# Optimization experiments

Hardware: AMD Instinct MI355X
Metric: run time of the kernel (lower is better)

Reference implementation:

```python
import jax, jax.numpy as jnp
import numpy as np

V, E, H, L, B, S = 50000, 512, 512, 2, 4, 256
DIN = 2 * E  # == 2*H, layer input size for all layers
GH = 4 * H   # torch LSTM gate order: i, f, g, o


def _lstm_dir(x, mask, w_ih, w_hh, b, reverse):
    """One direction of one LSTM layer with packed-sequence semantics.
    x: [B,S,DIN], mask: [B,S] bool. Returns [B,S,H]; padded steps emit 0
    and do not update state (matches pack_padded/pad_packed behavior)."""
    xs = jnp.swapaxes(x, 0, 1)                      # [S,B,DIN]
    ms = jnp.swapaxes(mask, 0, 1)[..., None]        # [S,B,1]
    pre = jnp.einsum('sbd,gd->sbg', xs, w_ih) + b   # input projection, [S,B,4H]

    def step(carry, inp):
        h, c = carry
        px, m = inp
        g = px + h @ w_hh.T
        i, f, gg, o = jnp.split(g, 4, axis=-1)
        c_new = jax.nn.sigmoid(f) * c + jax.nn.sigmoid(i) * jnp.tanh(gg)
        h_new = jax.nn.sigmoid(o) * jnp.tanh(c_new)
        h = jnp.where(m, h_new, h)
        c = jnp.where(m, c_new, c)
        return (h, c), jnp.where(m, h_new, jnp.zeros_like(h_new))

    init = (jnp.zeros((x.shape[0], H), x.dtype), jnp.zeros((x.shape[0], H), x.dtype))
    _, outs = jax.lax.scan(step, init, (pre, ms), reverse=reverse)
    return jnp.swapaxes(outs, 0, 1)                 # [B,S,H]


def setup_inputs() -> dict:
    key = jax.random.key(0)
    ks = jax.random.split(key, 12)
    sentence = jax.random.randint(ks[0], (B, S), 0, V)
    pos = jax.random.randint(ks[1], (B, S), 0, V)
    length = jax.random.randint(ks[2], (B,), S // 2, S + 1)
    length = length.at[0].set(S)  # ensure max(length) == S for static shapes
    emb = jax.random.normal(ks[3], (V, E), jnp.float32) * 0.02
    emb = emb.at[0].set(0.0)      # padding_idx row is zero
    sc = 1.0 / np.sqrt(H)
    w_ih = jax.random.uniform(ks[4], (L, 2, GH, DIN), jnp.float32, -sc, sc)
    w_hh = jax.random.uniform(ks[5], (L, 2, GH, H), jnp.float32, -sc, sc)
    b_ih = jax.random.uniform(ks[6], (L, 2, GH), jnp.float32, -sc, sc)
    b_hh = jax.random.uniform(ks[7], (L, 2, GH), jnp.float32, -sc, sc)
    s1 = 1.0 / np.sqrt(4 * H)
    w1 = jax.random.uniform(ks[8], (H, 4 * H), jnp.float32, -s1, s1)
    b1 = jax.random.uniform(ks[9], (H,), jnp.float32, -s1, s1)
    s2 = 1.0 / np.sqrt(H)
    w2 = jax.random.uniform(ks[10], (1, H), jnp.float32, -s2, s2)
    b2 = jax.random.uniform(ks[11], (1,), jnp.float32, -s2, s2)
    return {"sentence": sentence, "pos": pos, "length": length, "emb": emb,
            "w_ih": w_ih, "w_hh": w_hh, "b_ih": b_ih, "b_hh": b_hh,
            "w1": w1, "b1": b1, "w2": w2, "b2": b2}


def reference(sentence, pos, length, emb, w_ih, w_hh, b_ih, b_hh, w1, b1, w2, b2):
    x = jnp.concatenate([emb[sentence], emb[pos]], axis=-1)   # [B,S,2E]
    mask = jnp.arange(S)[None, :] < length[:, None]           # [B,S]
    for l in range(L):
        fwd = _lstm_dir(x, mask, w_ih[l, 0], w_hh[l, 0], b_ih[l, 0] + b_hh[l, 0], False)
        bwd = _lstm_dir(x, mask, w_ih[l, 1], w_hh[l, 1], b_ih[l, 1] + b_hh[l, 1], True)
        x = jnp.concatenate([fwd, bwd], axis=-1)              # [B,S,2H]
    # pairwise concat [feat_i ; feat_j] @ w1 == split w1 and broadcast-add
    wa, wb = w1[:, :2 * H], w1[:, 2 * H:]
    pa = jnp.einsum('bsd,hd->bsh', x, wa)                     # [B,S,H]
    pb = jnp.einsum('btd,hd->bth', x, wb)                     # [B,S,H]
    hmid = jnp.tanh(pa[:, :, None, :] + pb[:, None, :, :] + b1)  # [B,S,S,H]
    score = jnp.einsum('bsth,h->bst', hmid, w2[0]) + b2[0]    # [B,S,S]
    return score
```

## Files before the change

kernel.cpp:

```cpp
#include <hip/hip_runtime.h>

typedef unsigned int u32;
typedef unsigned short u16;
typedef unsigned long long u64;
typedef short bf16x8 __attribute__((ext_vector_type(8)));
typedef float f32x4 __attribute__((ext_vector_type(4)));

#define B_   4
#define S_   256
#define H_   512
#define GH_  2048
#define DIN_ 1024
#define M_   1024
#define WG_PER_DIR 32

__device__ __forceinline__ float bf2f(u16 u){
  union { u32 i; float f; } v; v.i = ((u32)u) << 16; return v.f;
}
__device__ __forceinline__ u16 f2bf(float f){
  union { float f; u32 i; } v; v.f = f;
  u32 r = v.i + 0x7fffu + ((v.i >> 16) & 1u);
  return (u16)(r >> 16);
}
__device__ __forceinline__ float sigm(float x){ return 1.f/(1.f + __expf(-x)); }
__device__ __forceinline__ float tanhfast(float x){
  float e = __expf(2.f*x); return 1.f - 2.f/(e + 1.f);
}
__device__ __forceinline__ void split8(const float* __restrict__ p,
                                       bf16x8& h, bf16x8& l){
  #pragma unroll
  for (int j = 0; j < 8; ++j){
    float f = p[j];
    u16 hh = f2bf(f);
    h[j] = (short)hh;
    l[j] = (short)f2bf(f - bf2f(hh));
  }
}

__global__ __launch_bounds__(256) void split_w(
    const float* __restrict__ src, u16* __restrict__ hi, u16* __restrict__ lo,
    int n4)
{
  int i = blockIdx.x*256 + threadIdx.x;
  if (i >= n4) return;
  float4 f = ((const float4*)src)[i];
  u16 h0 = f2bf(f.x), h1 = f2bf(f.y), h2 = f2bf(f.z), h3 = f2bf(f.w);
  u16 l0 = f2bf(f.x - bf2f(h0)), l1 = f2bf(f.y - bf2f(h1));
  u16 l2 = f2bf(f.z - bf2f(h2)), l3 = f2bf(f.w - bf2f(h3));
  ((u64*)hi)[i] = (u64)h0 | ((u64)h1<<16) | ((u64)h2<<32) | ((u64)h3<<48);
  ((u64*)lo)[i] = (u64)l0 | ((u64)l1<<16) | ((u64)l2<<32) | ((u64)l3<<48);
}

__global__ __launch_bounds__(256) void embed_kernel(
    const int* __restrict__ sent, const int* __restrict__ pos,
    const float* __restrict__ emb,
    u16* __restrict__ xhi, u16* __restrict__ xlo)
{
  const int m = blockIdx.x, tid = threadIdx.x;
  const int si = sent[m], pi = pos[m];
  const float2* es = (const float2*)(emb + (size_t)si * H_);
  const float2* ep = (const float2*)(emb + (size_t)pi * H_);
  float2 a = es[tid];
  float2 b = ep[tid];
  u32* xh = (u32*)(xhi + (size_t)m * DIN_);
  u32* xl = (u32*)(xlo + (size_t)m * DIN_);
  u16 ax = f2bf(a.x), ay = f2bf(a.y);
  u16 bx = f2bf(b.x), by = f2bf(b.y);
  xh[tid]       = (u32)ax | ((u32)ay << 16);
  xh[256 + tid] = (u32)bx | ((u32)by << 16);
  u16 axl = f2bf(a.x - bf2f(ax)), ayl = f2bf(a.y - bf2f(ay));
  u16 bxl = f2bf(b.x - bf2f(bx)), byl = f2bf(b.y - bf2f(by));
  xl[tid]       = (u32)axl | ((u32)ayl << 16);
  xl[256 + tid] = (u32)bxl | ((u32)byl << 16);
}

__global__ __launch_bounds__(256,2) void gemm_bf16(
    const u16* __restrict__ Ah, const u16* __restrict__ Al,
    const u16* __restrict__ Bh, const u16* __restrict__ Bl, int ldb, int perm,
    const float* __restrict__ bias1, const float* __restrict__ bias2,
    float* __restrict__ C, int N, int K)
{
  const int lane = threadIdx.x & 63, wave = threadIdx.x >> 6;
  const int m0 = blockIdx.y*64 + (wave>>1)*32;
  const int n0 = blockIdx.x*64 + (wave&1)*32;
  const int r15 = lane & 15, quad = lane >> 4;
  const u16* a0 = Ah + (size_t)(m0 + r15)*K + quad*8;
  const u16* a1 = a0 + (size_t)16*K;
  const u16* l0 = Al + (size_t)(m0 + r15)*K + quad*8;
  const u16* l1 = l0 + (size_t)16*K;
  const int nA = n0 + r15, nB = nA + 16;
  const int rA = perm ? ((nA&3)*H_ + (nA>>2)) : nA;
  const int rB = perm ? ((nB&3)*H_ + (nB>>2)) : nB;
  const u16* bh0 = Bh + (size_t)rA*ldb + quad*8;
  const u16* bh1 = Bh + (size_t)rB*ldb + quad*8;
  const u16* bl0 = Bl + (size_t)rA*ldb + quad*8;
  const u16* bl1 = Bl + (size_t)rB*ldb + quad*8;
  f32x4 acc00 = {0.f,0.f,0.f,0.f}, acc01 = acc00, acc10 = acc00, acc11 = acc00;
  for (int k = 0; k < K; k += 32){
    bf16x8 va0 = *(const bf16x8*)(a0 + k);
    bf16x8 va1 = *(const bf16x8*)(a1 + k);
    bf16x8 vl0 = *(const bf16x8*)(l0 + k);
    bf16x8 vl1 = *(const bf16x8*)(l1 + k);
    bf16x8 wh0 = *(const bf16x8*)(bh0 + k);
    bf16x8 wh1 = *(const bf16x8*)(bh1 + k);
    bf16x8 wl0v = *(const bf16x8*)(bl0 + k);
    bf16x8 wl1v = *(const bf16x8*)(bl1 + k);
    acc00 = __builtin_amdgcn_mfma_f32_16x16x32_bf16(va0, wh0, acc00, 0,0,0);
    acc00 = __builtin_amdgcn_mfma_f32_16x16x32_bf16(vl0, wh0, acc00, 0,0,0);
    acc00 = __builtin_amdgcn_mfma_f32_16x16x32_bf16(va0, wl0v, acc00, 0,0,0);
    acc01 = __builtin_amdgcn_mfma_f32_16x16x32_bf16(va0, wh1, acc01, 0,0,0);
    acc01 = __builtin_amdgcn_mfma_f32_16x16x32_bf16(vl0, wh1, acc01, 0,0,0);
    acc01 = __builtin_amdgcn_mfma_f32_16x16x32_bf16(va0, wl1v, acc01, 0,0,0);
    acc10 = __builtin_amdgcn_mfma_f32_16x16x32_bf16(va1, wh0, acc10, 0,0,0);
    acc10 = __builtin_amdgcn_mfma_f32_16x16x32_bf16(vl1, wh0, acc10, 0,0,0);
    acc10 = __builtin_amdgcn_mfma_f32_16x16x32_bf16(va1, wl0v, acc10, 0,0,0);
    acc11 = __builtin_amdgcn_mfma_f32_16x16x32_bf16(va1, wh1, acc11, 0,0,0);
    acc11 = __builtin_amdgcn_mfma_f32_16x16x32_bf16(vl1, wh1, acc11, 0,0,0);
    acc11 = __builtin_amdgcn_mfma_f32_16x16x32_bf16(va1, wl1v, acc11, 0,0,0);
  }
  float bA = 0.f, bB = 0.f;
  if (bias1){ bA += bias1[rA]; bB += bias1[rB]; }
  if (bias2){ bA += bias2[rA]; bB += bias2[rB]; }
  const int mr = m0 + quad*4;
  #pragma unroll
  for (int r = 0; r < 4; ++r){
    C[(size_t)(mr + r)*N + nA]      = acc00[r] + bA;
    C[(size_t)(mr + r)*N + nB]      = acc01[r] + bB;
    C[(size_t)(mr + r + 16)*N + nA] = acc10[r] + bA;
    C[(size_t)(mr + r + 16)*N + nB] = acc11[r] + bB;
  }
}

__global__ __launch_bounds__(256,2) void gemm_wT_x(
    const u16* __restrict__ Wh, const u16* __restrict__ Wl, int ldw,
    const u16* __restrict__ xh, const u16* __restrict__ xl,
    const float* __restrict__ biasM,
    float* __restrict__ CT, int K)
{
  const int lane = threadIdx.x & 63, wave = threadIdx.x >> 6;
  const int m0 = blockIdx.y*64 + (wave>>1)*32;
  const int n0 = blockIdx.x*64 + (wave&1)*32;
  const int b  = blockIdx.z;
  const int r15 = lane & 15, quad = lane >> 4;
  const u16* ah0 = Wh + (size_t)(m0 + r15)*ldw + quad*8;
  const u16* ah1 = ah0 + (size_t)16*ldw;
  const u16* al0 = Wl + (size_t)(m0 + r15)*ldw + quad*8;
  const u16* al1 = al0 + (size_t)16*ldw;
  const u16* bh0 = xh + (size_t)(b*S_ + n0 + r15)*DIN_ + quad*8;
  const u16* bh1 = bh0 + (size_t)16*DIN_;
  const u16* bl0 = xl + (size_t)(b*S_ + n0 + r15)*DIN_ + quad*8;
  const u16* bl1 = bl0 + (size_t)16*DIN_;
  f32x4 acc00 = {0.f,0.f,0.f,0.f}, acc01 = acc00, acc10 = acc00, acc11 = acc00;
  for (int k = 0; k < K; k += 32){
    bf16x8 vah0 = *(const bf16x8*)(ah0 + k);
    bf16x8 vah1 = *(const bf16x8*)(ah1 + k);
    bf16x8 val0 = *(const bf16x8*)(al0 + k);
    bf16x8 val1 = *(const bf16x8*)(al1 + k);
    bf16x8 vh0 = *(const bf16x8*)(bh0 + k);
    bf16x8 vh1 = *(const bf16x8*)(bh1 + k);
    bf16x8 vl0 = *(const bf16x8*)(bl0 + k);
    bf16x8 vl1 = *(const bf16x8*)(bl1 + k);
    acc00 = __builtin_amdgcn_mfma_f32_16x16x32_bf16(vah0, vh0, acc00, 0,0,0);
    acc00 = __builtin_amdgcn_mfma_f32_16x16x32_bf16(val0, vh0, acc00, 0,0,0);
    acc00 = __builtin_amdgcn_mfma_f32_16x16x32_bf16(vah0, vl0, acc00, 0,0,0);
    acc01 = __builtin_amdgcn_mfma_f32_16x16x32_bf16(vah0, vh1, acc01, 0,0,0);
    acc01 = __builtin_amdgcn_mfma_f32_16x16x32_bf16(val0, vh1, acc01, 0,0,0);
    acc01 = __builtin_amdgcn_mfma_f32_16x16x32_bf16(vah0, vl1, acc01, 0,0,0);
    acc10 = __builtin_amdgcn_mfma_f32_16x16x32_bf16(vah1, vh0, acc10, 0,0,0);
    acc10 = __builtin_amdgcn_mfma_f32_16x16x32_bf16(val1, vh0, acc10, 0,0,0);
    acc10 = __builtin_amdgcn_mfma_f32_16x16x32_bf16(vah1, vl0, acc10, 0,0,0);
    acc11 = __builtin_amdgcn_mfma_f32_16x16x32_bf16(vah1, vh1, acc11, 0,0,0);
    acc11 = __builtin_amdgcn_mfma_f32_16x16x32_bf16(val1, vh1, acc11, 0,0,0);
    acc11 = __builtin_amdgcn_mfma_f32_16x16x32_bf16(vah1, vl1, acc11, 0,0,0);
  }
  const int mr = m0 + quad*4;
  const int nA = n0 + r15, nB = nA + 16;
  #pragma unroll
  for (int r = 0; r < 4; ++r){
    float bia0 = biasM[mr + r];
    float bia1 = biasM[mr + r + 16];
    CT[(size_t)(b*H_ + mr + r)*S_ + nA]      = acc00[r] + bia0;
    CT[(size_t)(b*H_ + mr + r)*S_ + nB]      = acc01[r] + bia0;
    CT[(size_t)(b*H_ + mr + r + 16)*S_ + nA] = acc10[r] + bia1;
    CT[(size_t)(b*H_ + mr + r + 16)*S_ + nB] = acc11[r] + bia1;
  }
}

__global__ __launch_bounds__(256,1) void lstm_scan(
    const float* __restrict__ pre,
    const float* __restrict__ whh,
    const int* __restrict__ length,
    u32* __restrict__ Au32,
    u32* __restrict__ flags,
    u32* __restrict__ xh32, u32* __restrict__ xl32)
{
  const int wg = blockIdx.x;
  const int dir = wg >> 5, lwg = wg & 31;
  const int tid = threadIdx.x, lane = tid & 63, wave = tid >> 6;
  const int r15 = lane & 15, quad = lane >> 4;
  const int tile = lwg*4 + wave;
  const int gpbase = tile*16;

  const float* wdir = whh + (size_t)dir*GH_*H_;
  const int gp = gpbase + r15;
  const int srow = (gp & 3)*H_ + (gp >> 2);
  bf16x8 wh[16], wl[16];
  #pragma unroll
  for (int kk = 0; kk < 16; ++kk)
    split8(wdir + (size_t)srow*H_ + kk*32 + quad*8, wh[kk], wl[kk]);

  const float* preD = pre + (size_t)dir*M_*GH_;
  const int myb = lane & 3;
  const int njg = tile*4 + ((lane >> 2) & 3);
  const int lenb = length[myb];
  const int base = lane & ~3;
  const int row = r15 & 7;
  u32* AbufD = Au32 + dir*4096;
  u32* myflags = flags + dir*128;
  float h_state = 0.f, c_state = 0.f;

  float pcur[4];
  {
    const int s0 = dir ? (S_-1) : 0;
    #pragma unroll
    for (int r = 0; r < 4; ++r)
      pcur[r] = preD[(size_t)(r*S_ + s0)*GH_ + gpbase + r15];
  }

  for (int ss = 0; ss < S_; ++ss){
    const int s = dir ? (S_ - 1 - ss) : ss;
    const int rp = ss & 1;
    const u64* Ar64 = (const u64*)(AbufD + rp*2048);
    union { u64 d[2]; bf16x8 v; } ua[16];
    #pragma unroll
    for (int kk = 0; kk < 16; ++kk){
      ua[kk].d[0] = __hip_atomic_load(Ar64 + (size_t)row*128 + kk*8 + quad*2,
                                      __ATOMIC_RELAXED, __HIP_MEMORY_SCOPE_AGENT);
      ua[kk].d[1] = __hip_atomic_load(Ar64 + (size_t)row*128 + kk*8 + quad*2 + 1,
                                      __ATOMIC_RELAXED, __HIP_MEMORY_SCOPE_AGENT);
    }
    f32x4 a4[4];
    #pragma unroll
    for (int j = 0; j < 4; ++j) a4[j] = (f32x4){0.f,0.f,0.f,0.f};
    #pragma unroll
    for (int kk = 0; kk < 16; ++kk){
      const int j = kk >> 2;
      a4[j] = __builtin_amdgcn_mfma_f32_16x16x32_bf16(ua[kk].v, wh[kk], a4[j], 0,0,0);
      a4[j] = __builtin_amdgcn_mfma_f32_16x16x32_bf16(ua[kk].v, wl[kk], a4[j], 0,0,0);
    }
    f32x4 acc = (a4[0] + a4[1]) + (a4[2] + a4[3]);
    float si = 0.f, sf = 0.f, sg = 0.f, so = 0.f;
    #pragma unroll
    for (int r = 0; r < 4; ++r){
      float gsum = acc[r] + __shfl(acc[r], lane ^ 16);
      float gpre = gsum + pcur[r];
      float xi = __shfl(gpre, base + 0);
      float xf = __shfl(gpre, base + 1);
      float xg = __shfl(gpre, base + 2);
      float xo = __shfl(gpre, base + 3);
      if (r == myb){ si = xi; sf = xf; sg = xg; so = xo; }
    }
    float ctn = sigm(sf)*c_state + sigm(si)*tanhfast(sg);
    float htn = sigm(so)*tanhfast(ctn);
    const bool mk = (s < lenb);
    if (mk){ c_state = ctn; h_state = htn; }
    const float outv = mk ? htn : 0.f;
    if (ss + 1 < S_){
      const int sn = dir ? (S_ - 2 - ss) : (ss + 1);
      #pragma unroll
      for (int r = 0; r < 4; ++r)
        pcur[r] = preD[(size_t)(r*S_ + sn)*GH_ + gpbase + r15];
    }
    u32 hv = f2bf(h_state);
    u32 hl = f2bf(h_state - bf2f((u16)hv));
    u32 ov = f2bf(outv);
    u32 ol = f2bf(outv - bf2f((u16)ov));
    u32 ph  = (u32)__shfl((int)hv, lane ^ 4);
    u32 pl  = (u32)__shfl((int)hl, lane ^ 4);
    u32 po  = (u32)__shfl((int)ov, lane ^ 4);
    u32 pol = (u32)__shfl((int)ol, lane ^ 4);
    if (wave == 0 && lane < 16){
      u32* Aw = AbufD + (rp^1)*2048;
      const int p = njg >> 1;
      const int xw = (myb*S_ + s)*(DIN_/2) + dir*(H_/2) + p;
      if ((lane & 4) == 0){
        __hip_atomic_store(Aw + myb*256 + p, hv | (ph << 16),
                           __ATOMIC_RELAXED, __HIP_MEMORY_SCOPE_AGENT);
        xh32[xw] = ov | (po << 16);
      } else {
        __hip_atomic_store(Aw + (4+myb)*256 + p, pl | (hl << 16),
                           __ATOMIC_RELAXED, __HIP_MEMORY_SCOPE_AGENT);
        xl32[xw] = pol | (ol << 16);
      }
    } else if (wave != 0 && lane < 16){
      u32* Aw = AbufD + (rp^1)*2048;
      const int p = njg >> 1;
      const int xw = (myb*S_ + s)*(DIN_/2) + dir*(H_/2) + p;
      if ((lane & 4) == 0){
        __hip_atomic_store(Aw + myb*256 + p, hv | (ph << 16),
                           __ATOMIC_RELAXED, __HIP_MEMORY_SCOPE_AGENT);
        xh32[xw] = ov | (po << 16);
      } else {
        __hip_atomic_store(Aw + (4+myb)*256 + p, pl | (hl << 16),
                           __ATOMIC_RELAXED, __HIP_MEMORY_SCOPE_AGENT);
        xl32[xw] = pol | (ol << 16);
      }
    }
    if (ss != S_ - 1){
      __syncthreads();
      if (tid == 0)
        __hip_atomic_store(&myflags[lwg], (u32)(ss + 1),
                           __ATOMIC_RELAXED, __HIP_MEMORY_SCOPE_AGENT);
      if (wave == 0){
        const u32 tgt = (u32)(ss + 1);
        for (;;){
          u32 f = __hip_atomic_load(&myflags[lane & 31],
                                    __ATOMIC_RELAXED, __HIP_MEMORY_SCOPE_AGENT);
          if (__all((int)(f >= tgt))) break;
          __builtin_amdgcn_s_sleep(1);
        }
      }
      __syncthreads();
    }
  }
}

__global__ __launch_bounds__(256) void score_kernel(
    const float* __restrict__ pa, const float* __restrict__ pbT,
    const float* __restrict__ w2, const float* __restrict__ b2,
    float* __restrict__ out)
{
  const int bs = blockIdx.x;
  const int b = bs >> 8;
  const int t = threadIdx.x;
  __shared__ float pas[H_];
  __shared__ float w2s[H_];
  const float* paRow = pa + (size_t)bs*H_;
  for (int i = t; i < H_; i += 256){ pas[i] = paRow[i]; w2s[i] = w2[i]; }
  __syncthreads();
  const float* pbB = pbT + (size_t)b*H_*S_ + t;
  float acc = b2[0];
  #pragma unroll 4
  for (int h = 0; h < H_; ++h){
    float v = pas[h] + pbB[(size_t)h*S_];
    acc += w2s[h]*tanhfast(v);
  }
  out[(size_t)bs*S_ + t] = acc;
}

extern "C" void kernel_launch(void* const* d_in, const int* in_sizes, int n_in,
                              void* d_out, int out_size, void* d_ws, size_t ws_size,
                              hipStream_t stream)
{
  const int*   sent = (const int*)d_in[0];
  const int*   pos  = (const int*)d_in[1];
  const int*   len  = (const int*)d_in[2];
  const float* emb  = (const float*)d_in[3];
  const float* wih  = (const float*)d_in[4];
  const float* whh  = (const float*)d_in[5];
  const float* bih  = (const float*)d_in[6];
  const float* bhh  = (const float*)d_in[7];
  const float* w1   = (const float*)d_in[8];
  const float* b1   = (const float*)d_in[9];
  const float* w2   = (const float*)d_in[10];
  const float* b2   = (const float*)d_in[11];
  float* out = (float*)d_out;

  char* ws = (char*)d_ws;
  u32*   Au32  = (u32*)(ws);
  u32*   flags = (u32*)(ws + 32768);
  u16*   x0hi  = (u16*)(ws + ((size_t)1<<20));
  u16*   x0lo  = (u16*)(ws + ((size_t)3<<20));
  u16*   x1hi  = (u16*)(ws + ((size_t)5<<20));
  u16*   x1lo  = (u16*)(ws + ((size_t)7<<20));
  u16*   x2hi  = (u16*)(ws + ((size_t)9<<20));
  u16*   x2lo  = (u16*)(ws + ((size_t)11<<20));
  float* pa    = (float*)(ws + ((size_t)13<<20));
  float* pbT   = (float*)(ws + ((size_t)15<<20));
  float* pre   = (float*)(ws + ((size_t)17<<20));
  u16*   wihH  = (u16*)(ws + ((size_t)33<<20));
  u16*   wihL  = (u16*)(ws + ((size_t)49<<20));
  u16*   w1H   = (u16*)(ws + ((size_t)65<<20));
  u16*   w1L   = (u16*)(ws + ((size_t)67<<20));

  split_w<<<dim3(8192), dim3(256), 0, stream>>>(wih, wihH, wihL, 2097152);
  split_w<<<dim3(1024), dim3(256), 0, stream>>>(w1,  w1H,  w1L,   262144);

  embed_kernel<<<dim3(M_), dim3(256), 0, stream>>>(sent, pos, emb, x0hi, x0lo);

  for (int l = 0; l < 2; ++l){
    const u16* xh = l ? x1hi : x0hi;
    const u16* xl = l ? x1lo : x0lo;
    for (int d = 0; d < 2; ++d){
      const size_t wo = (size_t)(l*2+d)*GH_*DIN_;
      gemm_bf16<<<dim3(GH_/64, M_/64), dim3(256), 0, stream>>>(
        xh, xl, wihH + wo, wihL + wo, DIN_, 1,
        bih + (size_t)(l*2+d)*GH_, bhh + (size_t)(l*2+d)*GH_,
        pre + (size_t)d*M_*GH_, GH_, DIN_);
    }
    hipMemsetAsync(Au32, 0, 32768 + 1024, stream);
    u16* oh = l ? x2hi : x1hi;
    u16* ol = l ? x2lo : x1lo;
    lstm_scan<<<dim3(2*WG_PER_DIR), dim3(256), 0, stream>>>(
        pre, whh + (size_t)l*2*GH_*H_, len, Au32, flags, (u32*)oh, (u32*)ol);
  }

  gemm_bf16<<<dim3(H_/64, M_/64), dim3(256), 0, stream>>>(
      x2hi, x2lo, w1H, w1L, GH_, 0, nullptr, nullptr, pa, H_, DIN_);
  gemm_wT_x<<<dim3(S_/64, H_/64, B_), dim3(256), 0, stream>>>(
      w1H + DIN_, w1L + DIN_, GH_, x2hi, x2lo, b1, pbT, DIN_);
  score_kernel<<<dim3(M_), dim3(256), 0, stream>>>(pa, pbT, w2, b2, out);
}
```

Baseline: 3.302 ms.

## Replace flag barrier with step-tagged hidden-state records in LSTM scan

Each hidden-state word is now stored as a 64-bit record whose upper half carries the step number. Consumers spin on the data itself until every tag matches the expected step. This removes the per-step __syncthreads pair and the flag-array barrier across the 32 workgroups of each direction. In exchange it doubles the bytes of the recurrent buffer and makes each wave poll 64 atomic loads per retry, so both memory traffic and polling cost go up.

```diff
diff --git a/kernel.cpp b/kernel.cpp
--- a/kernel.cpp
+++ b/kernel.cpp
@@ -190,8 +190,7 @@
     const float* __restrict__ pre,
     const float* __restrict__ whh,
     const int* __restrict__ length,
-    u32* __restrict__ Au32,
-    u32* __restrict__ flags,
+    u64* __restrict__ Arec,
     u32* __restrict__ xh32, u32* __restrict__ xl32)
 {
   const int wg = blockIdx.x;
@@ -215,8 +214,7 @@
   const int lenb = length[myb];
   const int base = lane & ~3;
   const int row = r15 & 7;
-  u32* AbufD = Au32 + dir*4096;
-  u32* myflags = flags + dir*128;
+  u64* ArecD = Arec + dir*4096;
   float h_state = 0.f, c_state = 0.f;
 
   float pcur[4];
@@ -229,24 +227,35 @@
 
   for (int ss = 0; ss < S_; ++ss){
     const int s = dir ? (S_ - 1 - ss) : ss;
-    const int rp = ss & 1;
-    const u64* Ar64 = (const u64*)(AbufD + rp*2048);
-    union { u64 d[2]; bf16x8 v; } ua[16];
-    #pragma unroll
-    for (int kk = 0; kk < 16; ++kk){
-      ua[kk].d[0] = __hip_atomic_load(Ar64 + (size_t)row*128 + kk*8 + quad*2,
-                                      __ATOMIC_RELAXED, __HIP_MEMORY_SCOPE_AGENT);
-      ua[kk].d[1] = __hip_atomic_load(Ar64 + (size_t)row*128 + kk*8 + quad*2 + 1,
-                                      __ATOMIC_RELAXED, __HIP_MEMORY_SCOPE_AGENT);
+    const u64* Ar = ArecD + (size_t)(ss & 1)*2048 + (size_t)row*256;
+    const u32 Texp = (u32)ss;
+    u32 dat[16][4];
+    for (;;){
+      u32 bad = 0;
+      #pragma unroll
+      for (int kk = 0; kk < 16; ++kk){
+        #pragma unroll
+        for (int j = 0; j < 4; ++j){
+          u64 r = __hip_atomic_load(Ar + kk*16 + quad*4 + j,
+                                    __ATOMIC_RELAXED, __HIP_MEMORY_SCOPE_AGENT);
+          dat[kk][j] = (u32)r;
+          bad |= ((u32)(r >> 32)) ^ Texp;
+        }
+      }
+      if (__all(bad == 0)) break;
+      __builtin_amdgcn_s_sleep(1);
     }
     f32x4 a4[4];
     #pragma unroll
     for (int j = 0; j < 4; ++j) a4[j] = (f32x4){0.f,0.f,0.f,0.f};
     #pragma unroll
     for (int kk = 0; kk < 16; ++kk){
+      union { u32 w[4]; bf16x8 v; } u;
+      u.w[0] = dat[kk][0]; u.w[1] = dat[kk][1];
+      u.w[2] = dat[kk][2]; u.w[3] = dat[kk][3];
       const int j = kk >> 2;
-      a4[j] = __builtin_amdgcn_mfma_f32_16x16x32_bf16(ua[kk].v, wh[kk], a4[j], 0,0,0);
-      a4[j] = __builtin_amdgcn_mfma_f32_16x16x32_bf16(ua[kk].v, wl[kk], a4[j], 0,0,0);
+      a4[j] = __builtin_amdgcn_mfma_f32_16x16x32_bf16(u.v, wh[kk], a4[j], 0,0,0);
+      a4[j] = __builtin_amdgcn_mfma_f32_16x16x32_bf16(u.v, wl[kk], a4[j], 0,0,0);
     }
     f32x4 acc = (a4[0] + a4[1]) + (a4[2] + a4[3]);
     float si = 0.f, sf = 0.f, sg = 0.f, so = 0.f;
@@ -279,48 +288,20 @@
     u32 pl  = (u32)__shfl((int)hl, lane ^ 4);
     u32 po  = (u32)__shfl((int)ov, lane ^ 4);
     u32 pol = (u32)__shfl((int)ol, lane ^ 4);
-    if (wave == 0 && lane < 16){
-      u32* Aw = AbufD + (rp^1)*2048;
+    if (lane < 16){
+      u64* Aw = ArecD + (size_t)((ss + 1) & 1)*2048;
+      const u64 tag = ((u64)(u32)(ss + 1)) << 32;
       const int p = njg >> 1;
       const int xw = (myb*S_ + s)*(DIN_/2) + dir*(H_/2) + p;
       if ((lane & 4) == 0){
-        __hip_atomic_store(Aw + myb*256 + p, hv | (ph << 16),
+        __hip_atomic_store(Aw + myb*256 + p, tag | (u64)(hv | (ph << 16)),
                            __ATOMIC_RELAXED, __HIP_MEMORY_SCOPE_AGENT);
         xh32[xw] = ov | (po << 16);
       } else {
-        __hip_atomic_store(Aw + (4+myb)*256 + p, pl | (hl << 16),
+        __hip_atomic_store(Aw + (4+myb)*256 + p, tag | (u64)(pl | (hl << 16)),
                            __ATOMIC_RELAXED, __HIP_MEMORY_SCOPE_AGENT);
         xl32[xw] = pol | (ol << 16);
       }
-    } else if (wave != 0 && lane < 16){
-      u32* Aw = AbufD + (rp^1)*2048;
-      const int p = njg >> 1;
-      const int xw = (myb*S_ + s)*(DIN_/2) + dir*(H_/2) + p;
-      if ((lane & 4) == 0){
-        __hip_atomic_store(Aw + myb*256 + p, hv | (ph << 16),
-                           __ATOMIC_RELAXED, __HIP_MEMORY_SCOPE_AGENT);
-        xh32[xw] = ov | (po << 16);
-      } else {
-        __hip_atomic_store(Aw + (4+myb)*256 + p, pl | (hl << 16),
-                           __ATOMIC_RELAXED, __HIP_MEMORY_SCOPE_AGENT);
-        xl32[xw] = pol | (ol << 16);
-      }
-    }
-    if (ss != S_ - 1){
-      __syncthreads();
-      if (tid == 0)
-        __hip_atomic_store(&myflags[lwg], (u32)(ss + 1),
-                           __ATOMIC_RELAXED, __HIP_MEMORY_SCOPE_AGENT);
-      if (wave == 0){
-        const u32 tgt = (u32)(ss + 1);
-        for (;;){
-          u32 f = __hip_atomic_load(&myflags[lane & 31],
-                                    __ATOMIC_RELAXED, __HIP_MEMORY_SCOPE_AGENT);
-          if (__all((int)(f >= tgt))) break;
-          __builtin_amdgcn_s_sleep(1);
-        }
-      }
-      __syncthreads();
     }
   }
 }
@@ -367,8 +348,7 @@
   float* out = (float*)d_out;
 
   char* ws = (char*)d_ws;
-  u32*   Au32  = (u32*)(ws);
-  u32*   flags = (u32*)(ws + 32768);
+  u64*   Arec  = (u64*)(ws);
   u16*   x0hi  = (u16*)(ws + ((size_t)1<<20));
   u16*   x0lo  = (u16*)(ws + ((size_t)3<<20));
   u16*   x1hi  = (u16*)(ws + ((size_t)5<<20));
@@ -398,11 +378,11 @@
         bih + (size_t)(l*2+d)*GH_, bhh + (size_t)(l*2+d)*GH_,
         pre + (size_t)d*M_*GH_, GH_, DIN_);
     }
-    hipMemsetAsync(Au32, 0, 32768 + 1024, stream);
+    hipMemsetAsync(Arec, 0, 65536, stream);
     u16* oh = l ? x2hi : x1hi;
     u16* ol = l ? x2lo : x1lo;
     lstm_scan<<<dim3(2*WG_PER_DIR), dim3(256), 0, stream>>>(
-        pre, whh + (size_t)l*2*GH_*H_, len, Au32, flags, (u32*)oh, (u32*)ol);
+        pre, whh + (size_t)l*2*GH_*H_, len, Arec, (u32*)oh, (u32*)ol);
   }
 
   gemm_bf16<<<dim3(H_/64, M_/64), dim3(256), 0, stream>>>(
```

After: 11.92 ms. 261% more time.
